# Optimization experiments

Hardware: AMD Instinct MI355X
Metric: run time of the kernel (lower is better)

The kernel has to match this reference:

```python
import jax, jax.numpy as jnp
import numpy as np

# Static config matching init_kwargs
H = 12            # num_heads
ALPHA = (1, 2, 3)
DEPTH = 5
BLOCK_DEPTH = 3
TOTAL_DEPTH_M1 = 14 - 1   # total_depth - 1
SMALL_ACTIVE = (BLOCK_DEPTH <= DEPTH <= TOTAL_DEPTH_M1 - BLOCK_DEPTH)  # True here


def _ln(x, g, b, eps=1e-5):
    m = jnp.mean(x, axis=-1, keepdims=True)
    v = jnp.mean((x - m) ** 2, axis=-1, keepdims=True)
    return (x - m) * jax.lax.rsqrt(v + eps) * g + b


def _attn_branch(xp, w_qkv, w_proj, b_proj, keep_heads, keep_ch):
    # xp: (B2, N, C). Heads >= keep_heads are zeroed in q,k,v (as in the torch
    # clone+zero), output channels >= keep_ch zeroed after proj.
    B2, N, C = xp.shape
    hd = C // H
    scale = hd ** -0.5
    qkv = (xp @ w_qkv).reshape(B2, N, 3, H, hd).transpose(2, 0, 3, 1, 4)  # (3,B2,H,N,hd)
    hmask = (jnp.arange(H) < keep_heads).astype(xp.dtype)[None, :, None, None]
    q, k, v = qkv[0] * hmask, qkv[1] * hmask, qkv[2] * hmask
    a = jax.nn.softmax(jnp.einsum('bhnd,bhmd->bhnm', q, k) * scale, axis=-1)
    o = jnp.einsum('bhnm,bhmd->bhnd', a, v).transpose(0, 2, 1, 3).reshape(B2, N, C)
    o = o @ w_proj + b_proj
    cmask = (jnp.arange(C) < keep_ch).astype(xp.dtype)
    return o * cmask


def _mlp_branch(xp, w1, b1, w2, b2, keep_ch):
    # Input channels >= keep_ch zeroed before fc1, output channels zeroed after fc2.
    C = xp.shape[-1]
    cmask = (jnp.arange(C) < keep_ch).astype(xp.dtype)
    h = jax.nn.gelu((xp * cmask) @ w1 + b1, approximate=False)  # torch nn.GELU exact
    return ((h @ w2) + b2) * cmask


def setup_inputs() -> dict:
    key = jax.random.key(0)
    ks = jax.random.split(key, 8)
    B, N, C = 64, 257, 768
    HID = 4 * C

    def w(k, shape):
        return jax.random.normal(k, shape, jnp.float32) * 0.02

    return {
        'x': jax.random.normal(ks[0], (B, N, C), jnp.float32),
        'gumbel_weights': jax.random.uniform(ks[1], (3,), jnp.float32),
        'n1l_g': jnp.ones((C,), jnp.float32), 'n1l_b': jnp.zeros((C,), jnp.float32),
        'n1s_g': jnp.ones((C,), jnp.float32), 'n1s_b': jnp.zeros((C,), jnp.float32),
        'w_qkv': w(ks[2], (C, 3 * C)),  # qkv_bias=False
        'w_proj': w(ks[3], (C, C)), 'b_proj': jnp.zeros((C,), jnp.float32),
        'n2l_g': jnp.ones((C,), jnp.float32), 'n2l_b': jnp.zeros((C,), jnp.float32),
        'n2s_g': jnp.ones((C,), jnp.float32), 'n2s_b': jnp.zeros((C,), jnp.float32),
        'w_fc1': w(ks[4], (C, HID)), 'b_fc1': jnp.zeros((HID,), jnp.float32),
        'w_fc2': w(ks[5], (HID, C)), 'b_fc2': jnp.zeros((C,), jnp.float32),
    }


def reference(x, gumbel_weights, n1l_g, n1l_b, n1s_g, n1s_b, w_qkv, w_proj, b_proj,
              n2l_g, n2l_b, n2s_g, n2s_b, w_fc1, b_fc1, w_fc2, b_fc2):
    B, N, C = x.shape
    B2 = B // 2

    # --- attention sub-block (pre-norm, residual) ---
    nl = _ln(x[:B2], n1l_g, n1l_b)
    ns = _ln(x[B2:], n1s_g, n1s_b)
    a_large = _attn_branch(nl, w_qkv, w_proj, b_proj, H, C)
    if SMALL_ACTIVE:
        a_small = sum(
            gumbel_weights[i] * _attn_branch(ns, w_qkv, w_proj, b_proj,
                                             H // ALPHA[i], C // ALPHA[i])
            for i in range(3))
        attn_out = jnp.concatenate([a_large, a_small], axis=0)
    else:
        attn_out = jnp.concatenate([a_large, a_large], axis=0)
    x = x + attn_out  # drop_path = Identity

    # --- mlp sub-block (pre-norm, residual) ---
    nl2 = _ln(x[:B2], n2l_g, n2l_b)
    ns2 = _ln(x[B2:], n2s_g, n2s_b)
    m_large = _mlp_branch(nl2, w_fc1, b_fc1, w_fc2, b_fc2, C)
    if SMALL_ACTIVE:
        m_small = sum(
            gumbel_weights[i] * _mlp_branch(ns2, w_fc1, b_fc1, w_fc2, b_fc2,
                                            C // ALPHA[i])
            for i in range(3))
        mlp_out = jnp.concatenate([m_large, m_small], axis=0)
    else:
        mlp_out = jnp.concatenate([m_large, m_large], axis=0)
    return x + mlp_out
```

## Files before the change

kernel.cpp:

```cpp
#include <hip/hip_runtime.h>
#include <hip/hip_bf16.h>

typedef short v8s __attribute__((ext_vector_type(8)));
typedef float v4f __attribute__((ext_vector_type(4)));

#define B2ROWS 8224
#define ROWS   16448

__global__ __launch_bounds__(256) void wprep(const float* __restrict__ W,
                                             __hip_bfloat16* __restrict__ Wt,
                                             int K, int N, int variant,
                                             const float* __restrict__ gw) {
  int k = blockIdx.x * 256 + threadIdx.x;
  int n = blockIdx.y;
  if (k >= K) return;
  float v = W[(size_t)k * N + n];
  if (variant == 1) {
    int h = k >> 6;
    float s = gw[0];
    if (h < 6 && n < 384) s += gw[1];
    if (h < 4 && n < 256) s += gw[2];
    v *= s;
  }
  Wt[(size_t)n * K + k] = __float2bfloat16(v);
}

__global__ void bias_prep(const float* __restrict__ bp, const float* __restrict__ b2,
                          const float* __restrict__ gw,
                          float* __restrict__ b_small, float* __restrict__ b2_small) {
  int c = blockIdx.x * 256 + threadIdx.x;
  if (c >= 768) return;
  float s = gw[0] + (c < 384 ? gw[1] : 0.f) + (c < 256 ? gw[2] : 0.f);
  b_small[c] = bp[c] * s;
  b2_small[c] = b2[c] * s;
}

__global__ __launch_bounds__(256) void ln_k(const float* __restrict__ X,
                                            __hip_bfloat16* __restrict__ out,
                                            const float* __restrict__ gl, const float* __restrict__ bl,
                                            const float* __restrict__ gs, const float* __restrict__ bs) {
  int wave = threadIdx.x >> 6, lane = threadIdx.x & 63;
  int row = blockIdx.x * 4 + wave;
  const float* g = (row < B2ROWS) ? gl : gs;
  const float* b = (row < B2ROWS) ? bl : bs;
  const float* xr = X + (size_t)row * 768;
  float v[12]; float s = 0.f, ss = 0.f;
#pragma unroll
  for (int i = 0; i < 12; i++) { v[i] = xr[lane + i * 64]; s += v[i]; ss += v[i] * v[i]; }
#pragma unroll
  for (int o = 32; o > 0; o >>= 1) { s += __shfl_xor(s, o, 64); ss += __shfl_xor(ss, o, 64); }
  float mean = s * (1.0f / 768.0f);
  float var = ss * (1.0f / 768.0f) - mean * mean;
  float rstd = rsqrtf(var + 1e-5f);
  __hip_bfloat16* orow = out + (size_t)row * 768;
#pragma unroll
  for (int i = 0; i < 12; i++) {
    int c = lane + i * 64;
    orow[c] = __float2bfloat16((v[i] - mean) * rstd * g[c] + b[c]);
  }
}

__global__ __launch_bounds__(256) void gemm_k(
    const __hip_bfloat16* __restrict__ A, int lda,
    const __hip_bfloat16* __restrict__ Bt, int ldb,
    int M, int K,
    const float* __restrict__ bias,
    const float* __restrict__ resid, int ldr,
    const float* __restrict__ gw, int gidx,
    const __hip_bfloat16* __restrict__ addin,
    void* __restrict__ out, int ldo,
    int mode) {
  __shared__ __attribute__((aligned(16))) short As[3][128 * 32];
  __shared__ __attribute__((aligned(16))) short Bs[3][128 * 32];
  int tid = threadIdx.x;
  int lane = tid & 63;
  int wave = tid >> 6;
  int wm = wave >> 1, wn = wave & 1;
  int l16 = lane & 15, quad = lane >> 4;
  int m0 = blockIdx.y * 128, n0 = blockIdx.x * 128;
  int sw = (quad ^ ((l16 >> 1) & 3)) * 8;

  int r4 = lane >> 2;
  int qs = (lane & 3) ^ ((r4 >> 1) & 3);

  const ushort* Au = (const ushort*)A;
  const ushort* Bu = (const ushort*)Bt;

  const ushort* agp[2];
  const ushort* bgp[2];
  int lof[2];
#pragma unroll
  for (int it = 0; it < 2; it++) {
    int rbase = wave * 16 + it * 64;
    int gr = m0 + rbase + r4; if (gr > M - 1) gr = M - 1;
    agp[it] = Au + (size_t)gr * lda + qs * 8;
    int gn = n0 + rbase + r4;
    bgp[it] = Bu + (size_t)gn * ldb + qs * 8;
    lof[it] = rbase * 32;
  }

  v4f acc[4][4];
#pragma unroll
  for (int i = 0; i < 4; i++)
#pragma unroll
    for (int j = 0; j < 4; j++) acc[i][j] = (v4f){0.f, 0.f, 0.f, 0.f};

  auto stage = [&](int buf, int ko) {
#pragma unroll
    for (int it = 0; it < 2; it++) {
      __builtin_amdgcn_global_load_lds(
          (const __attribute__((address_space(1))) uint32_t*)(uintptr_t)(const void*)(agp[it] + ko),
          (__attribute__((address_space(3))) uint32_t*)(uint32_t)(uintptr_t)(const void*)&As[buf][lof[it]],
          16, 0, 0);
      __builtin_amdgcn_global_load_lds(
          (const __attribute__((address_space(1))) uint32_t*)(uintptr_t)(const void*)(bgp[it] + ko),
          (__attribute__((address_space(3))) uint32_t*)(uint32_t)(uintptr_t)(const void*)&Bs[buf][lof[it]],
          16, 0, 0);
    }
  };

  int nk = K >> 5;
  stage(0, 0);
  stage(1, 32);

  int bc = 0;
  for (int t = 0; t < nk; ++t) {
    __builtin_amdgcn_sched_barrier(0);
    if (t + 1 < nk) {
      asm volatile("s_waitcnt vmcnt(4)" ::: "memory");
    } else {
      asm volatile("s_waitcnt vmcnt(0)" ::: "memory");
    }
    __builtin_amdgcn_s_barrier();
    __builtin_amdgcn_sched_barrier(0);
    if (t + 2 < nk) {
      int bsg = bc - 1; if (bsg < 0) bsg += 3;
      stage(bsg, (t + 2) * 32);
    }
    v8s af[4], bfr[4];
#pragma unroll
    for (int i = 0; i < 4; i++) af[i] = *(const v8s*)&As[bc][(wm * 64 + i * 16 + l16) * 32 + sw];
#pragma unroll
    for (int j = 0; j < 4; j++) bfr[j] = *(const v8s*)&Bs[bc][(wn * 64 + j * 16 + l16) * 32 + sw];
#pragma unroll
    for (int i = 0; i < 4; i++)
#pragma unroll
      for (int j = 0; j < 4; j++)
        acc[i][j] = __builtin_amdgcn_mfma_f32_16x16x32_bf16(af[i], bfr[j], acc[i][j], 0, 0, 0);
    bc++; if (bc == 3) bc = 0;
  }

  float scale = (gidx >= 0) ? gw[gidx] : 1.0f;

  __syncthreads();
  char* sbase = ((wave < 2) ? (char*)As : (char*)Bs) + (wave & 1) * 12288;

  if (mode != 2) {
    ushort* S16 = (ushort*)sbase;
#pragma unroll
    for (int i = 0; i < 4; i++) {
#pragma unroll
      for (int j = 0; j < 4; j++) {
        int gc = n0 + wn * 64 + j * 16 + l16;
#pragma unroll
        for (int r = 0; r < 4; r++) {
          float v = acc[i][j][r];
          if (mode == 1) {
            float z = v + bias[gc];
            v = scale * (0.5f * z * (1.0f + erff(z * 0.70710678118654752f)));
          }
          __hip_bfloat16 hb = __float2bfloat16(v);
          S16[(i * 16 + quad * 4 + r) * 72 + j * 16 + l16] = *(const ushort*)&hb;
        }
      }
    }
    asm volatile("s_waitcnt lgkmcnt(0)" ::: "memory");
#pragma unroll
    for (int rr = 0; rr < 8; rr++) {
      int row = rr * 8 + (lane >> 3);
      int col0 = (lane & 7) * 8;
      int gr = m0 + wm * 64 + row;
      v8s val = *(const v8s*)&S16[row * 72 + col0];
      if (gr < M) {
        size_t go = (size_t)gr * ldo + (n0 + wn * 64 + col0);
        if (mode == 1 && addin) {
          v8s av = *(const v8s*)&((const ushort*)addin)[go];
#pragma unroll
          for (int e = 0; e < 8; e++) {
            float fv = __uint_as_float(((uint)(ushort)val[e]) << 16);
            float fa = __uint_as_float(((uint)(ushort)av[e]) << 16);
            __hip_bfloat16 hr = __float2bfloat16(fv + fa);
            val[e] = *(const short*)&hr;
          }
        }
        *(v8s*)&((ushort*)out)[go] = val;
      }
    }
  } else {
    float* S32 = (float*)sbase;
#pragma unroll
    for (int h = 0; h < 2; h++) {
      if (h) asm volatile("s_waitcnt lgkmcnt(0)" ::: "memory");
#pragma unroll
      for (int i = 0; i < 4; i++) {
#pragma unroll
        for (int jj = 0; jj < 2; jj++) {
          int j = h * 2 + jj;
          int gc = n0 + wn * 64 + j * 16 + l16;
#pragma unroll
          for (int r = 0; r < 4; r++)
            S32[(i * 16 + quad * 4 + r) * 36 + jj * 16 + l16] = acc[i][j][r] + bias[gc];
        }
      }
      asm volatile("s_waitcnt lgkmcnt(0)" ::: "memory");
#pragma unroll
      for (int rr = 0; rr < 8; rr++) {
        int row = rr * 8 + (lane >> 3);
        int c0 = (lane & 7) * 4;
        int gr = m0 + wm * 64 + row;
        v4f v = *(const v4f*)&S32[row * 36 + c0];
        if (gr < M) {
          int gc0 = n0 + wn * 64 + h * 32 + c0;
          v4f rv = *(const v4f*)&resid[(size_t)gr * ldr + gc0];
          v4f sres = v + rv;
          *(v4f*)&((float*)out)[(size_t)gr * ldo + gc0] = sres;
        }
      }
    }
  }
}

__global__ __launch_bounds__(256) void attn_k(const __hip_bfloat16* __restrict__ qkv,
                                              __hip_bfloat16* __restrict__ O) {
  __shared__ ushort Ks[64 * 72];
  __shared__ ushort Vs[64 * 64];
  __shared__ ushort Ps[4][16 * 72];
  int bh = blockIdx.x;
  int b = bh / 12, h = bh % 12;
  size_t base = (size_t)b * 257;
  const ushort* Qg = (const ushort*)qkv;
  int tid = threadIdx.x;
  int w = tid >> 6, lane = tid & 63;
  int l16 = lane & 15, quad = lane >> 4;
  int qrow0 = blockIdx.y * 64 + w * 16;

  v8s aq[2];
  {
    int gr = qrow0 + l16; if (gr > 256) gr = 256;
    const ushort* qp = Qg + (base + gr) * 2304 + h * 64;
    aq[0] = *(const v8s*)(qp + quad * 8);
    aq[1] = *(const v8s*)(qp + 32 + quad * 8);
  }

  float mrow[4], lrow[4];
  v4f o[4];
#pragma unroll
  for (int r = 0; r < 4; r++) { mrow[r] = -1e30f; lrow[r] = 0.f; }
#pragma unroll
  for (int dt = 0; dt < 4; dt++) o[dt] = (v4f){0.f, 0.f, 0.f, 0.f};

  for (int kt = 0; kt < 5; kt++) {
    __syncthreads();
#pragma unroll
    for (int it = 0; it < 2; it++) {
      int ch = tid + it * 256;
      int row = ch >> 3, oct = ch & 7;
      int gk = kt * 64 + row; if (gk > 256) gk = 256;
      *(uint4*)&Ks[row * 72 + oct * 8] =
        *(const uint4*)(Qg + (base + gk) * 2304 + 768 + h * 64 + oct * 8);
    }
#pragma unroll
    for (int it = 0; it < 2; it++) {
      int oct = w + it * 4;
      int gk = kt * 64 + lane; if (gk > 256) gk = 256;
      ushort tmp[8];
      *(uint4*)tmp = *(const uint4*)(Qg + (base + gk) * 2304 + 1536 + h * 64 + oct * 8);
#pragma unroll
      for (int j = 0; j < 8; j++) {
        int d = oct * 8 + j;
        Vs[d * 64 + (((lane >> 3) ^ j) * 8) + (lane & 7)] = tmp[j];
      }
    }
    __syncthreads();

    v4f s[4];
#pragma unroll
    for (int jt = 0; jt < 4; jt++) {
      v8s bk0 = *(const v8s*)&Ks[(jt * 16 + l16) * 72 + quad * 8];
      v8s bk1 = *(const v8s*)&Ks[(jt * 16 + l16) * 72 + 32 + quad * 8];
      v4f acc = (v4f){0.f, 0.f, 0.f, 0.f};
      acc = __builtin_amdgcn_mfma_f32_16x16x32_bf16(aq[0], bk0, acc, 0, 0, 0);
      acc = __builtin_amdgcn_mfma_f32_16x16x32_bf16(aq[1], bk1, acc, 0, 0, 0);
      s[jt] = acc;
    }
#pragma unroll
    for (int jt = 0; jt < 4; jt++) {
      int col = kt * 64 + jt * 16 + l16;
      bool valid = col < 257;
#pragma unroll
      for (int r = 0; r < 4; r++)
        s[jt][r] = valid ? s[jt][r] * 0.125f : -1e30f;
    }
    float mnew[4], alpha[4], psum[4];
#pragma unroll
    for (int r = 0; r < 4; r++) {
      float mx = fmaxf(fmaxf(s[0][r], s[1][r]), fmaxf(s[2][r], s[3][r]));
#pragma unroll
      for (int off = 1; off < 16; off <<= 1) mx = fmaxf(mx, __shfl_xor(mx, off, 64));
      mnew[r] = fmaxf(mrow[r], mx);
      alpha[r] = __expf(mrow[r] - mnew[r]);
      mrow[r] = mnew[r];
      psum[r] = 0.f;
    }
#pragma unroll
    for (int jt = 0; jt < 4; jt++) {
#pragma unroll
      for (int r = 0; r < 4; r++) {
        float p = __expf(s[jt][r] - mnew[r]);
        psum[r] += p;
        __hip_bfloat16 pb = __float2bfloat16(p);
        Ps[w][(quad * 4 + r) * 72 + jt * 16 + l16] = *(ushort*)&pb;
      }
    }
#pragma unroll
    for (int r = 0; r < 4; r++) {
#pragma unroll
      for (int off = 1; off < 16; off <<= 1) psum[r] += __shfl_xor(psum[r], off, 64);
      lrow[r] = lrow[r] * alpha[r] + psum[r];
    }
#pragma unroll
    for (int dt = 0; dt < 4; dt++)
#pragma unroll
      for (int r = 0; r < 4; r++) o[dt][r] *= alpha[r];
    v8s pa0 = *(const v8s*)&Ps[w][l16 * 72 + quad * 8];
    v8s pa1 = *(const v8s*)&Ps[w][l16 * 72 + 32 + quad * 8];
#pragma unroll
    for (int dt = 0; dt < 4; dt++) {
      int d = dt * 16 + l16;
      v8s bv0 = *(const v8s*)&Vs[d * 64 + ((quad ^ (d & 7)) * 8)];
      v8s bv1 = *(const v8s*)&Vs[d * 64 + (((4 + quad) ^ (d & 7)) * 8)];
      o[dt] = __builtin_amdgcn_mfma_f32_16x16x32_bf16(pa0, bv0, o[dt], 0, 0, 0);
      o[dt] = __builtin_amdgcn_mfma_f32_16x16x32_bf16(pa1, bv1, o[dt], 0, 0, 0);
    }
  }
#pragma unroll
  for (int r = 0; r < 4; r++) {
    int gr = qrow0 + quad * 4 + r;
    if (gr < 257) {
      float inv = 1.f / lrow[r];
      __hip_bfloat16* orow = O + (base + gr) * 768 + h * 64;
#pragma unroll
      for (int dt = 0; dt < 4; dt++)
        orow[dt * 16 + l16] = __float2bfloat16(o[dt][r] * inv);
    }
  }
}

extern "C" void kernel_launch(void* const* d_in, const int* in_sizes, int n_in,
                              void* d_out, int out_size, void* d_ws, size_t ws_size,
                              hipStream_t stream) {
  const float* x      = (const float*)d_in[0];
  const float* gw     = (const float*)d_in[1];
  const float* n1l_g  = (const float*)d_in[2];
  const float* n1l_b  = (const float*)d_in[3];
  const float* n1s_g  = (const float*)d_in[4];
  const float* n1s_b  = (const float*)d_in[5];
  const float* w_qkv  = (const float*)d_in[6];
  const float* w_proj = (const float*)d_in[7];
  const float* b_proj = (const float*)d_in[8];
  const float* n2l_g  = (const float*)d_in[9];
  const float* n2l_b  = (const float*)d_in[10];
  const float* n2s_g  = (const float*)d_in[11];
  const float* n2s_b  = (const float*)d_in[12];
  const float* w_fc1  = (const float*)d_in[13];
  const float* b_fc1  = (const float*)d_in[14];
  const float* w_fc2  = (const float*)d_in[15];
  const float* b_fc2  = (const float*)d_in[16];
  float* out = (float*)d_out;

  const size_t REQUIRED = (size_t)(2304*768 + 2*768*768 + 2*3072*768) * 2
                        + 2 * 768 * 4 + 512
                        + (size_t)ROWS * 768 * 2
                        + (size_t)ROWS * 2304 * 2;
  if (ws_size < REQUIRED) return;

  char* ws = (char*)d_ws;
  size_t off = 0;
  auto alloc = [&](size_t bytes) -> void* {
    void* p = ws + off;
    off = (off + bytes + 255) & ~(size_t)255;
    return p;
  };
  __hip_bfloat16* wqkv_t  = (__hip_bfloat16*)alloc((size_t)2304 * 768 * 2);
  __hip_bfloat16* wproj_l = (__hip_bfloat16*)alloc((size_t)768 * 768 * 2);
  __hip_bfloat16* wproj_s = (__hip_bfloat16*)alloc((size_t)768 * 768 * 2);
  __hip_bfloat16* wfc1_t  = (__hip_bfloat16*)alloc((size_t)3072 * 768 * 2);
  __hip_bfloat16* wfc2_t  = (__hip_bfloat16*)alloc((size_t)768 * 3072 * 2);
  float* b_small  = (float*)alloc(768 * 4);
  float* b2_small = (float*)alloc(768 * 4);
  __hip_bfloat16* xn   = (__hip_bfloat16*)alloc((size_t)ROWS * 768 * 2);
  __hip_bfloat16* qkv  = (__hip_bfloat16*)alloc((size_t)ROWS * 2304 * 2);
  __hip_bfloat16* Obuf = xn;
  __hip_bfloat16* xn2  = qkv;
  __hip_bfloat16* hbuf = qkv + (size_t)ROWS * 768;

  wprep<<<dim3(3, 2304), 256, 0, stream>>>(w_qkv, wqkv_t, 768, 2304, 0, gw);
  wprep<<<dim3(3, 768),  256, 0, stream>>>(w_proj, wproj_l, 768, 768, 0, gw);
  wprep<<<dim3(3, 768),  256, 0, stream>>>(w_proj, wproj_s, 768, 768, 1, gw);
  wprep<<<dim3(3, 3072), 256, 0, stream>>>(w_fc1, wfc1_t, 768, 3072, 0, gw);
  wprep<<<dim3(12, 768), 256, 0, stream>>>(w_fc2, wfc2_t, 3072, 768, 0, gw);
  bias_prep<<<3, 256, 0, stream>>>(b_proj, b_fc2, gw, b_small, b2_small);

  ln_k<<<ROWS / 4, 256, 0, stream>>>(x, xn, n1l_g, n1l_b, n1s_g, n1s_b);

  gemm_k<<<dim3(18, 129), 256, 0, stream>>>(xn, 768, wqkv_t, 768, ROWS, 768,
                                            nullptr, nullptr, 0, gw, -1, nullptr,
                                            qkv, 2304, 0);
  attn_k<<<dim3(768, 5), 256, 0, stream>>>(qkv, Obuf);

  gemm_k<<<dim3(6, 65), 256, 0, stream>>>(Obuf, 768, wproj_l, 768, B2ROWS, 768,
                                          b_proj, x, 768, gw, -1, nullptr, out, 768, 2);
  gemm_k<<<dim3(6, 65), 256, 0, stream>>>(Obuf + (size_t)B2ROWS * 768, 768, wproj_s, 768, B2ROWS, 768,
                                          b_small, x + (size_t)B2ROWS * 768, 768, gw, -1, nullptr,
                                          out + (size_t)B2ROWS * 768, 768, 2);

  ln_k<<<ROWS / 4, 256, 0, stream>>>(out, xn2, n2l_g, n2l_b, n2s_g, n2s_b);
  const __hip_bfloat16* xn2s = xn2 + (size_t)B2ROWS * 768;
  float* outs = out + (size_t)B2ROWS * 768;

  gemm_k<<<dim3(24, 65), 256, 0, stream>>>(xn2, 768, wfc1_t, 768, B2ROWS, 768,
                                           b_fc1, nullptr, 0, gw, -1, nullptr, hbuf, 3072, 1);
  gemm_k<<<dim3(6, 65), 256, 0, stream>>>(hbuf, 3072, wfc2_t, 3072, B2ROWS, 3072,
                                          b_fc2, out, 768, gw, -1, nullptr, out, 768, 2);

  gemm_k<<<dim3(24, 65), 256, 0, stream>>>(xn2s, 768, wfc1_t, 768, B2ROWS, 768,
                                           b_fc1, nullptr, 0, gw, 0, nullptr, hbuf, 3072, 1);
  gemm_k<<<dim3(3, 65), 256, 0, stream>>>(hbuf, 3072, wfc2_t + (size_t)384 * 3072, 3072, B2ROWS, 3072,
                                          b2_small + 384, outs + 384, 768, gw, -1, nullptr, outs + 384, 768, 2);
  gemm_k<<<dim3(24, 65), 256, 0, stream>>>(xn2s, 768, wfc1_t, 768, B2ROWS, 384,
                                           b_fc1, nullptr, 0, gw, 1, hbuf, hbuf, 3072, 1);
  gemm_k<<<dim3(1, 65), 256, 0, stream>>>(hbuf, 3072, wfc2_t + (size_t)256 * 3072, 3072, B2ROWS, 3072,
                                          b2_small + 256, outs + 256, 768, gw, -1, nullptr, outs + 256, 768, 2);
  gemm_k<<<dim3(24, 65), 256, 0, stream>>>(xn2s, 768, wfc1_t, 768, B2ROWS, 256,
                                           b_fc1, nullptr, 0, gw, 2, hbuf, hbuf, 3072, 1);
  gemm_k<<<dim3(2, 65), 256, 0, stream>>>(hbuf, 3072, wfc2_t, 3072, B2ROWS, 3072,
                                          b2_small, outs, 768, gw, -1, nullptr, outs, 768, 2);
}
```

Before: 886.8 us.

## Fuse small-branch fc1 prefixes into one pass, XCD-remap tiles, use fast erf

```diff
diff --git a/kernel.cpp b/kernel.cpp
--- a/kernel.cpp
+++ b/kernel.cpp
@@ -6,6 +6,18 @@
 
 #define B2ROWS 8224
 #define ROWS   16448
+
+__device__ __forceinline__ float fast_gelu(float z) {
+  float u = z * 0.70710678118654752f;
+  float a = fabsf(u);
+  float t = __builtin_amdgcn_rcpf(1.0f + 0.3275911f * a);
+  float p = t * (0.254829592f + t * (-0.284496736f + t * (1.421413741f +
+            t * (-1.453152027f + t * 1.061405429f))));
+  float e = __expf(-a * a);
+  float erfa = 1.0f - p * e;
+  float erfu = copysignf(erfa, u);
+  return 0.5f * z * (1.0f + erfu);
+}
 
 __global__ __launch_bounds__(256) void wprep(const float* __restrict__ W,
                                              __hip_bfloat16* __restrict__ Wt,
@@ -60,7 +72,8 @@
   }
 }
 
-__global__ __launch_bounds__(256) void gemm_k(
+template<int FUSED>
+__device__ __forceinline__ void gemm_body(
     const __hip_bfloat16* __restrict__ A, int lda,
     const __hip_bfloat16* __restrict__ Bt, int ldb,
     int M, int K,
@@ -69,21 +82,38 @@
     const float* __restrict__ gw, int gidx,
     const __hip_bfloat16* __restrict__ addin,
     void* __restrict__ out, int ldo,
-    int mode) {
-  __shared__ __attribute__((aligned(16))) short As[3][128 * 32];
-  __shared__ __attribute__((aligned(16))) short Bs[3][128 * 32];
+    int mode,
+    __hip_bfloat16* __restrict__ aux1,
+    __hip_bfloat16* __restrict__ aux2) {
+  __shared__ __attribute__((aligned(16))) short Asm[3][128 * 32];
+  __shared__ __attribute__((aligned(16))) short Bsm[3][128 * 32];
   int tid = threadIdx.x;
   int lane = tid & 63;
   int wave = tid >> 6;
   int wm = wave >> 1, wn = wave & 1;
   int l16 = lane & 15, quad = lane >> 4;
-  int m0 = blockIdx.y * 128, n0 = blockIdx.x * 128;
+
+  int gx = gridDim.x;
+  int nwg = gx * gridDim.y;
+  int bid = blockIdx.y * gx + blockIdx.x;
+  int q8 = nwg >> 3, r8 = nwg & 7;
+  int xcd = bid & 7, lid = bid >> 3;
+  int nb = (xcd < r8 ? xcd * (q8 + 1) : r8 * (q8 + 1) + (xcd - r8) * q8) + lid;
+  int m0 = (nb / gx) * 128, n0 = (nb % gx) * 128;
+
   int sw = (quad ^ ((l16 >> 1) & 3)) * 8;
+
+  const __hip_bfloat16* Ause = A;
+  if (!FUSED && mode == 4) {
+    if (n0 < 256) Ause = aux2;
+    else if (n0 < 384) Ause = aux1;
+    mode = 2;
+  }
 
   int r4 = lane >> 2;
   int qs = (lane & 3) ^ ((r4 >> 1) & 3);
 
-  const ushort* Au = (const ushort*)A;
+  const ushort* Au = (const ushort*)Ause;
   const ushort* Bu = (const ushort*)Bt;
 
   const ushort* agp[2];
@@ -105,16 +135,40 @@
 #pragma unroll
     for (int j = 0; j < 4; j++) acc[i][j] = (v4f){0.f, 0.f, 0.f, 0.f};
 
+  float bias4[4];
+  float gw0 = 0.f, gw1 = 0.f, gw2 = 0.f;
+  uint g1p[4][4][2], g2p[4][4][2];
+  if constexpr (FUSED) {
+    gw0 = gw[0]; gw1 = gw[1]; gw2 = gw[2];
+#pragma unroll
+    for (int j = 0; j < 4; j++) bias4[j] = bias[n0 + wn * 64 + j * 16 + l16];
+  }
+
+  auto snap = [&](uint (&gp)[4][4][2], float gwX) {
+#pragma unroll
+    for (int i = 0; i < 4; i++)
+#pragma unroll
+      for (int j = 0; j < 4; j++)
+#pragma unroll
+        for (int p = 0; p < 2; p++) {
+          float v0 = gwX * fast_gelu(acc[i][j][2 * p] + bias4[j]);
+          float v1 = gwX * fast_gelu(acc[i][j][2 * p + 1] + bias4[j]);
+          __hip_bfloat16 h0 = __float2bfloat16(v0);
+          __hip_bfloat16 h1 = __float2bfloat16(v1);
+          gp[i][j][p] = ((uint)*(const ushort*)&h1 << 16) | (uint)*(const ushort*)&h0;
+        }
+  };
+
   auto stage = [&](int buf, int ko) {
 #pragma unroll
     for (int it = 0; it < 2; it++) {
       __builtin_amdgcn_global_load_lds(
           (const __attribute__((address_space(1))) uint32_t*)(uintptr_t)(const void*)(agp[it] + ko),
-          (__attribute__((address_space(3))) uint32_t*)(uint32_t)(uintptr_t)(const void*)&As[buf][lof[it]],
+          (__attribute__((address_space(3))) uint32_t*)(uint32_t)(uintptr_t)(const void*)&Asm[buf][lof[it]],
           16, 0, 0);
       __builtin_amdgcn_global_load_lds(
           (const __attribute__((address_space(1))) uint32_t*)(uintptr_t)(const void*)(bgp[it] + ko),
-          (__attribute__((address_space(3))) uint32_t*)(uint32_t)(uintptr_t)(const void*)&Bs[buf][lof[it]],
+          (__attribute__((address_space(3))) uint32_t*)(uint32_t)(uintptr_t)(const void*)&Bsm[buf][lof[it]],
           16, 0, 0);
     }
   };
@@ -125,6 +179,10 @@
 
   int bc = 0;
   for (int t = 0; t < nk; ++t) {
+    if constexpr (FUSED) {
+      if (t == 8)  snap(g2p, gw2);
+      if (t == 12) snap(g1p, gw1);
+    }
     __builtin_amdgcn_sched_barrier(0);
     if (t + 1 < nk) {
       asm volatile("s_waitcnt vmcnt(4)" ::: "memory");
@@ -139,9 +197,9 @@
     }
     v8s af[4], bfr[4];
 #pragma unroll
-    for (int i = 0; i < 4; i++) af[i] = *(const v8s*)&As[bc][(wm * 64 + i * 16 + l16) * 32 + sw];
-#pragma unroll
-    for (int j = 0; j < 4; j++) bfr[j] = *(const v8s*)&Bs[bc][(wn * 64 + j * 16 + l16) * 32 + sw];
+    for (int i = 0; i < 4; i++) af[i] = *(const v8s*)&Asm[bc][(wm * 64 + i * 16 + l16) * 32 + sw];
+#pragma unroll
+    for (int j = 0; j < 4; j++) bfr[j] = *(const v8s*)&Bsm[bc][(wn * 64 + j * 16 + l16) * 32 + sw];
 #pragma unroll
     for (int i = 0; i < 4; i++)
 #pragma unroll
@@ -150,10 +208,71 @@
     bc++; if (bc == 3) bc = 0;
   }
 
+  if constexpr (FUSED) {
+#pragma unroll
+    for (int i = 0; i < 4; i++)
+#pragma unroll
+      for (int j = 0; j < 4; j++)
+#pragma unroll
+        for (int r = 0; r < 4; r++)
+          acc[i][j][r] = gw0 * fast_gelu(acc[i][j][r] + bias4[j]);
+
+    __syncthreads();
+    ushort* S16 = (ushort*)(((wave < 2) ? (char*)Asm : (char*)Bsm) + (wave & 1) * 12288);
+
+    auto flush = [&](void* dst) {
+      asm volatile("s_waitcnt lgkmcnt(0)" ::: "memory");
+#pragma unroll
+      for (int i = 0; i < 4; i++)
+#pragma unroll
+        for (int j = 0; j < 4; j++)
+#pragma unroll
+          for (int r = 0; r < 4; r++) {
+            __hip_bfloat16 hb = __float2bfloat16(acc[i][j][r]);
+            S16[(i * 16 + quad * 4 + r) * 72 + j * 16 + l16] = *(const ushort*)&hb;
+          }
+      asm volatile("s_waitcnt lgkmcnt(0)" ::: "memory");
+#pragma unroll
+      for (int rr = 0; rr < 8; rr++) {
+        int row = rr * 8 + (lane >> 3);
+        int col0 = (lane & 7) * 8;
+        int gr = m0 + wm * 64 + row;
+        v8s val = *(const v8s*)&S16[row * 72 + col0];
+        if (gr < M)
+          *(v8s*)&((ushort*)dst)[(size_t)gr * ldo + (n0 + wn * 64 + col0)] = val;
+      }
+    };
+
+    flush(out);
+#pragma unroll
+    for (int i = 0; i < 4; i++)
+#pragma unroll
+      for (int j = 0; j < 4; j++)
+#pragma unroll
+        for (int p = 0; p < 2; p++) {
+          uint u = g1p[i][j][p];
+          acc[i][j][2 * p]     += __uint_as_float(u << 16);
+          acc[i][j][2 * p + 1] += __uint_as_float(u & 0xffff0000u);
+        }
+    flush(aux1);
+#pragma unroll
+    for (int i = 0; i < 4; i++)
+#pragma unroll
+      for (int j = 0; j < 4; j++)
+#pragma unroll
+        for (int p = 0; p < 2; p++) {
+          uint u = g2p[i][j][p];
+          acc[i][j][2 * p]     += __uint_as_float(u << 16);
+          acc[i][j][2 * p + 1] += __uint_as_float(u & 0xffff0000u);
+        }
+    flush(aux2);
+    return;
+  } else {
+
   float scale = (gidx >= 0) ? gw[gidx] : 1.0f;
 
   __syncthreads();
-  char* sbase = ((wave < 2) ? (char*)As : (char*)Bs) + (wave & 1) * 12288;
+  char* sbase = ((wave < 2) ? (char*)Asm : (char*)Bsm) + (wave & 1) * 12288;
 
   if (mode != 2) {
     ushort* S16 = (ushort*)sbase;
@@ -167,7 +286,7 @@
           float v = acc[i][j][r];
           if (mode == 1) {
             float z = v + bias[gc];
-            v = scale * (0.5f * z * (1.0f + erff(z * 0.70710678118654752f)));
+            v = scale * fast_gelu(z);
           }
           __hip_bfloat16 hb = __float2bfloat16(v);
           S16[(i * 16 + quad * 4 + r) * 72 + j * 16 + l16] = *(const ushort*)&hb;
@@ -228,6 +347,36 @@
       }
     }
   }
+  }
+}
+
+__global__ __launch_bounds__(256) void gemm_k(
+    const __hip_bfloat16* __restrict__ A, int lda,
+    const __hip_bfloat16* __restrict__ Bt, int ldb,
+    int M, int K,
+    const float* __restrict__ bias,
+    const float* __restrict__ resid, int ldr,
+    const float* __restrict__ gw, int gidx,
+    const __hip_bfloat16* __restrict__ addin,
+    void* __restrict__ out, int ldo,
+    int mode,
+    __hip_bfloat16* __restrict__ aux1,
+    __hip_bfloat16* __restrict__ aux2) {
+  gemm_body<0>(A, lda, Bt, ldb, M, K, bias, resid, ldr, gw, gidx, addin,
+               out, ldo, mode, aux1, aux2);
+}
+
+__global__ __launch_bounds__(256) void fc1f_k(
+    const __hip_bfloat16* __restrict__ A, int lda,
+    const __hip_bfloat16* __restrict__ Bt, int ldb,
+    int M, int K,
+    const float* __restrict__ bias,
+    const float* __restrict__ gw,
+    void* __restrict__ out, int ldo,
+    __hip_bfloat16* __restrict__ outB,
+    __hip_bfloat16* __restrict__ outC) {
+  gemm_body<1>(A, lda, Bt, ldb, M, K, bias, nullptr, 0, gw, -1, nullptr,
+               out, ldo, 3, outB, outC);
 }
 
 __global__ __launch_bounds__(256) void attn_k(const __hip_bfloat16* __restrict__ qkv,
@@ -404,6 +553,14 @@
   __hip_bfloat16* xn2  = qkv;
   __hip_bfloat16* hbuf = qkv + (size_t)ROWS * 768;
 
+  const size_t HB2 = (size_t)B2ROWS * 3072 * 2;
+  bool roomy = ws_size >= REQUIRED + 2 * HB2 + 512;
+  __hip_bfloat16 *outB = nullptr, *outC = nullptr;
+  if (roomy) {
+    outB = (__hip_bfloat16*)alloc(HB2);
+    outC = (__hip_bfloat16*)alloc(HB2);
+  }
+
   wprep<<<dim3(3, 2304), 256, 0, stream>>>(w_qkv, wqkv_t, 768, 2304, 0, gw);
   wprep<<<dim3(3, 768),  256, 0, stream>>>(w_proj, wproj_l, 768, 768, 0, gw);
   wprep<<<dim3(3, 768),  256, 0, stream>>>(w_proj, wproj_s, 768, 768, 1, gw);
@@ -415,34 +572,51 @@
 
   gemm_k<<<dim3(18, 129), 256, 0, stream>>>(xn, 768, wqkv_t, 768, ROWS, 768,
                                             nullptr, nullptr, 0, gw, -1, nullptr,
-                                            qkv, 2304, 0);
+                                            qkv, 2304, 0, nullptr, nullptr);
   attn_k<<<dim3(768, 5), 256, 0, stream>>>(qkv, Obuf);
 
   gemm_k<<<dim3(6, 65), 256, 0, stream>>>(Obuf, 768, wproj_l, 768, B2ROWS, 768,
-                                          b_proj, x, 768, gw, -1, nullptr, out, 768, 2);
+                                          b_proj, x, 768, gw, -1, nullptr, out, 768, 2,
+                                          nullptr, nullptr);
   gemm_k<<<dim3(6, 65), 256, 0, stream>>>(Obuf + (size_t)B2ROWS * 768, 768, wproj_s, 768, B2ROWS, 768,
                                           b_small, x + (size_t)B2ROWS * 768, 768, gw, -1, nullptr,
-                                          out + (size_t)B2ROWS * 768, 768, 2);
+                                          out + (size_t)B2ROWS * 768, 768, 2, nullptr, nullptr);
 
   ln_k<<<ROWS / 4, 256, 0, stream>>>(out, xn2, n2l_g, n2l_b, n2s_g, n2s_b);
   const __hip_bfloat16* xn2s = xn2 + (size_t)B2ROWS * 768;
   float* outs = out + (size_t)B2ROWS * 768;
 
   gemm_k<<<dim3(24, 65), 256, 0, stream>>>(xn2, 768, wfc1_t, 768, B2ROWS, 768,
-                                           b_fc1, nullptr, 0, gw, -1, nullptr, hbuf, 3072, 1);
+                                           b_fc1, nullptr, 0, gw, -1, nullptr, hbuf, 3072, 1,
+                                           nullptr, nullptr);
   gemm_k<<<dim3(6, 65), 256, 0, stream>>>(hbuf, 3072, wfc2_t, 3072, B2ROWS, 3072,
-                                          b_fc2, out, 768, gw, -1, nullptr, out, 768, 2);
-
-  gemm_k<<<dim3(24, 65), 256, 0, stream>>>(xn2s, 768, wfc1_t, 768, B2ROWS, 768,
-                                           b_fc1, nullptr, 0, gw, 0, nullptr, hbuf, 3072, 1);
-  gemm_k<<<dim3(3, 65), 256, 0, stream>>>(hbuf, 3072, wfc2_t + (size_t)384 * 3072, 3072, B2ROWS, 3072,
-                                          b2_small + 384, outs + 384, 768, gw, -1, nullptr, outs + 384, 768, 2);
-  gemm_k<<<dim3(24, 65), 256, 0, stream>>>(xn2s, 768, wfc1_t, 768, B2ROWS, 384,
-                                           b_fc1, nullptr, 0, gw, 1, hbuf, hbuf, 3072, 1);
-  gemm_k<<<dim3(1, 65), 256, 0, stream>>>(hbuf, 3072, wfc2_t + (size_t)256 * 3072, 3072, B2ROWS, 3072,
-                                          b2_small + 256, outs + 256, 768, gw, -1, nullptr, outs + 256, 768, 2);
-  gemm_k<<<dim3(24, 65), 256, 0, stream>>>(xn2s, 768, wfc1_t, 768, B2ROWS, 256,
-                                           b_fc1, nullptr, 0, gw, 2, hbuf, hbuf, 3072, 1);
-  gemm_k<<<dim3(2, 65), 256, 0, stream>>>(hbuf, 3072, wfc2_t, 3072, B2ROWS, 3072,
-                                          b2_small, outs, 768, gw, -1, nullptr, outs, 768, 2);
-}
+                                          b_fc2, out, 768, gw, -1, nullptr, out, 768, 2,
+                                          nullptr, nullptr);
+
+  if (roomy) {
+    fc1f_k<<<dim3(24, 65), 256, 0, stream>>>(xn2s, 768, wfc1_t, 768, B2ROWS, 768,
+                                             b_fc1, gw, hbuf, 3072, outB, outC);
+    gemm_k<<<dim3(6, 65), 256, 0, stream>>>(hbuf, 3072, wfc2_t, 3072, B2ROWS, 3072,
+                                            b2_small, outs, 768, gw, -1, nullptr, outs, 768, 4,
+                                            outB, outC);
+  } else {
+    gemm_k<<<dim3(24, 65), 256, 0, stream>>>(xn2s, 768, wfc1_t, 768, B2ROWS, 768,
+                                             b_fc1, nullptr, 0, gw, 0, nullptr, hbuf, 3072, 1,
+                                             nullptr, nullptr);
+    gemm_k<<<dim3(3, 65), 256, 0, stream>>>(hbuf, 3072, wfc2_t + (size_t)384 * 3072, 3072, B2ROWS, 3072,
+                                            b2_small + 384, outs + 384, 768, gw, -1, nullptr, outs + 384, 768, 2,
+                                            nullptr, nullptr);
+    gemm_k<<<dim3(24, 65), 256, 0, stream>>>(xn2s, 768, wfc1_t, 768, B2ROWS, 384,
+                                             b_fc1, nullptr, 0, gw, 1, hbuf, hbuf, 3072, 1,
+                                             nullptr, nullptr);
+    gemm_k<<<dim3(1, 65), 256, 0, stream>>>(hbuf, 3072, wfc2_t + (size_t)256 * 3072, 3072, B2ROWS, 3072,
+                                            b2_small + 256, outs + 256, 768, gw, -1, nullptr, outs + 256, 768, 2,
+                                            nullptr, nullptr);
+    gemm_k<<<dim3(24, 65), 256, 0, stream>>>(xn2s, 768, wfc1_t, 768, B2ROWS, 256,
+                                             b_fc1, nullptr, 0, gw, 2, hbuf, hbuf, 3072, 1,
+                                             nullptr, nullptr);
+    gemm_k<<<dim3(2, 65), 256, 0, stream>>>(hbuf, 3072, wfc2_t, 3072, B2ROWS, 3072,
+                                            b2_small, outs, 768, gw, -1, nullptr, outs, 768, 2,
+                                            nullptr, nullptr);
+  }
+}
```

Result: faster. 745.2 us (-16.0%).
